# Kernel optimization log

Hardware: AMD Instinct MI355X
Metric: run time of the kernel (lower is better)

The kernel has to match this reference:

```python
import jax, jax.numpy as jnp
import numpy as np

S = (256, 256, 256)          # MRI volume shape
N = 50000                    # number of Gaussians
T = 16                       # fixed tile edge; covers max bbox width = 2*3*sigma_max*(S-1)+2 <= 15
SIG_MIN, SIG_MAX = 0.004, 0.008  # NN-distance-based sigma range (k_sigma=1)


def setup_inputs() -> dict:
    key = jax.random.key(0)
    k1, k2, k3 = jax.random.split(key, 3)
    centers = jax.random.uniform(k1, (N, 3), dtype=jnp.float32)
    sigmas = jax.random.uniform(k2, (N,), dtype=jnp.float32, minval=SIG_MIN, maxval=SIG_MAX)
    intensities = jax.random.uniform(k3, (N,), dtype=jnp.float32)
    return {"centers": centers, "sigmas": sigmas, "intensities": intensities}


def _splat(centers, sigmas, intensities):
    dt = centers.dtype
    scale = jnp.asarray([s - 1 for s in S], dtype=dt)            # (3,) == scale_factors
    shape_f = jnp.asarray(S, dtype=dt)                           # (3,)
    shape_i = jnp.asarray(S, dtype=jnp.int32)                    # (3,)

    center_vox = centers * scale                                 # (N,3) voxel-space centers
    cutoff = 3.0 * sigmas[:, None] * scale                       # (N,3)
    # original: min_idx = max(c-cut, 0).int(); max_idx = (min(c+cut, scale)+1).int(), clipped to S
    min_idx = jnp.floor(jnp.maximum(center_vox - cutoff, 0.0)).astype(jnp.int32)          # (N,3)
    max_idx = jnp.minimum(jnp.floor(jnp.minimum(center_vox + cutoff, scale)) + 1.0,
                          shape_f).astype(jnp.int32)             # (N,3), exclusive

    ar = jnp.arange(T, dtype=jnp.int32)
    idx = min_idx[:, :, None] + ar[None, None, :]                # (N,3,T) absolute voxel idx
    valid = idx < max_idx[:, :, None]                            # (N,3,T) inside variable bbox
    idx_c = jnp.minimum(idx, shape_i[None, :, None] - 1)         # clamp for safe gather/scatter

    # grid coordinate along axis a at voxel i is i/(S_a-1) (linspace(0,1,S_a))
    coord = idx_c.astype(dt) / scale[None, :, None]              # (N,3,T)
    d = coord - centers[:, :, None]                              # (N,3,T)
    d2 = (d[:, 0, :, None, None] ** 2
          + d[:, 1, None, :, None] ** 2
          + d[:, 2, None, None, :] ** 2)                         # (N,T,T,T)
    mask = (valid[:, 0, :, None, None]
            & valid[:, 1, None, :, None]
            & valid[:, 2, None, None, :])                        # (N,T,T,T)

    inv_two_sig2 = 0.5 / (sigmas * sigmas)                       # (N,)
    contrib = intensities[:, None, None, None] * jnp.exp(-d2 * inv_two_sig2[:, None, None, None])
    contrib = jnp.where(mask, contrib, jnp.zeros((), dt))        # (N,T,T,T)

    lin = (idx_c[:, 0, :, None, None] * (S[1] * S[2])
           + idx_c[:, 1, None, :, None] * S[2]
           + idx_c[:, 2, None, None, :])                         # (N,T,T,T) flat voxel index

    vol = jnp.zeros(S[0] * S[1] * S[2], dtype=dt)
    vol = vol.at[lin.reshape(-1)].add(contrib.reshape(-1))
    return vol.reshape(S)


def reference(centers, sigmas, intensities):
    return _splat(centers, sigmas, intensities)
```

## Files before the change

### kernel.cpp

```cpp
#include <hip/hip_runtime.h>


#define NTILE 32768
#define CAP   32
#define LOG2E 1.4426950408889634f

typedef unsigned long long ull;

struct __align__(16) Rec {
    float cy, cz, w2;
    unsigned meta;
    float ex[8];
};

__global__ __launch_bounds__(256) void bin_prep_kernel(
    const float* __restrict__ centers,
    const float* __restrict__ sigmas,
    const float* __restrict__ intens,
    int*  __restrict__ counts,
    Rec*  __restrict__ list,
    int N)
{
    int g = blockIdx.x * 256 + threadIdx.x;
    if (g >= N) return;
    int txi = blockIdx.y % 3;
    int tyi = blockIdx.y / 3;

    float cx = centers[3*g+0] * 255.0f;
    float cy = centers[3*g+1] * 255.0f;
    float cz = centers[3*g+2] * 255.0f;
    float sig = sigmas[g];
    float cut = 3.0f * sig * 255.0f;
    float cc[3] = {cx, cy, cz};
    int mn[3], mx[3];
    #pragma unroll
    for (int a = 0; a < 3; ++a) {
        mn[a] = (int)floorf(fmaxf(cc[a] - cut, 0.0f));
        mx[a] = (int)fminf(floorf(fminf(cc[a] + cut, 255.0f)) + 1.0f, 256.0f);
    }
    float s255 = sig * 255.0f;
    float w2 = -0.5f * LOG2E / (s255 * s255);
    float inten = intens[g];

    int t0x = mn[0] >> 3, t1x = (mx[0] - 1) >> 3;
    int t0y = mn[1] >> 3, t1y = (mx[1] - 1) >> 3;

    int tx = t0x + txi; if (tx > t1x) return;
    int ty = t0y + tyi; if (ty > t1y) return;

    int ox = tx << 3, oy = ty << 3;
    int lox = max(mn[0] - ox, 0), hix = min(mx[0] - ox, 8);
    int loy = max(mn[1] - oy, 0), hiy = min(mx[1] - oy, 8);

    float ex[8];
    #pragma unroll
    for (int i = 0; i < 8; ++i) {
        float d = (float)(ox + i) - cx;
        float v = exp2f(d * d * w2) * inten;
        ex[i] = (i >= lox && i < hix) ? v : 0.0f;
    }

    int tzc = ((int)cz) >> 3;
    int t = (tx << 10) | (ty << 5) | tzc;
    unsigned meta = (unsigned)mn[2] | ((unsigned)(mx[2] - 1) << 8)
                  | ((unsigned)loy << 16) | ((unsigned)hiy << 19);

    int slot = atomicAdd(&counts[t], 1);
    if (slot < CAP) {
        int4* p = (int4*)&list[(size_t)t * CAP + slot];
        p[0] = make_int4(__float_as_int(cy), __float_as_int(cz),
                         __float_as_int(w2), (int)meta);
        p[1] = make_int4(__float_as_int(ex[0]), __float_as_int(ex[1]),
                         __float_as_int(ex[2]), __float_as_int(ex[3]));
        p[2] = make_int4(__float_as_int(ex[4]), __float_as_int(ex[5]),
                         __float_as_int(ex[6]), __float_as_int(ex[7]));
    }
}

__global__ __launch_bounds__(256) void splat_main(
    const int*  __restrict__ counts,
    const Rec*  __restrict__ list,
    float* __restrict__ vol)
{
    __shared__ int4 sh[4][(3 * CAP + 2) * 3];

    int wid = threadIdx.x >> 6;
    int lane = threadIdx.x & 63;
    int t = __builtin_amdgcn_readfirstlane(blockIdx.x * 4 + wid);
    int ox = (t >> 10) << 3, oy = ((t >> 5) & 31) << 3, oz = (t & 31) << 3;
    int tz = t & 31;
    int ly = lane >> 3, lz = lane & 7;

    int c0 = (tz > 0)  ? counts[t - 1] : 0;  if (c0 > CAP) c0 = CAP;
    int c1 = counts[t];                       if (c1 > CAP) c1 = CAP;
    int c2 = (tz < 31) ? counts[t + 1] : 0;  if (c2 > CAP) c2 = CAP;
    int n01 = c0 + c1, ntot = n01 + c2;

    const int4* s0 = (const int4*)(list + (long)(t - 1) * CAP);
    const int4* s1 = (const int4*)(list + (long)t * CAP);
    const int4* s2 = (const int4*)(list + (long)(t + 1) * CAP);

    int e0 = 3 * c0, e1 = 3 * n01, etot = 3 * ntot;
    for (int k = lane; k < etot; k += 64) {
        const int4* src; int off;
        if (k < e0)      { src = s0; off = k; }
        else if (k < e1) { src = s1; off = k - e0; }
        else             { src = s2; off = k - e1; }
        sh[wid][k] = src[off];
    }

    float fy = (float)(oy + ly);
    float fz = (float)(oz + lz);

    float acc[8];
    #pragma unroll
    for (int i = 0; i < 8; ++i) acc[i] = 0.0f;

    const int4* P = sh[wid];

    int4 a0 = P[0], a1 = P[1], a2 = P[2];
    for (int k = 0; k < ntot; ++k) {
        int b = (k + 1) * 3;
        int4 b0 = P[b], b1 = P[b + 1], b2 = P[b + 2];

        unsigned meta = (unsigned)__builtin_amdgcn_readfirstlane(a0.w);
        int mnz  = (int)(meta & 0xFF);
        int mxzi = (int)((meta >> 8) & 0xFF);
        int loz = mnz - oz;      if (loz < 0) loz = 0;
        int hiz = mxzi + 1 - oz; if (hiz > 8) hiz = 8;
        if (loz < hiz) {
            int loy_ = (int)((meta >> 16) & 7);
            int hiy_ = (int)((meta >> 19) & 0xF);
            ull ym = ((~0ull) << (loy_ << 3)) & ((~0ull) >> (64 - (hiy_ << 3)));
            unsigned zpat = (0xFFu >> (8 - hiz)) & (0xFFu << loz);
            unsigned zrep = zpat * 0x01010101u;
            ull m = (((ull)zrep << 32) | (ull)zrep) & ym;

            float cyv = __int_as_float(a0.x), czv = __int_as_float(a0.y);
            float w2v = __int_as_float(a0.z);

            float dy = fy - cyv, dz = fz - czv;
            float e = exp2f(fmaf(dy, dy, dz * dz) * w2v);
            float em;
            asm("v_cndmask_b32 %0, 0, %1, %2" : "=v"(em) : "v"(e), "s"(m));

            acc[0] = fmaf(__int_as_float(a1.x), em, acc[0]);
            acc[1] = fmaf(__int_as_float(a1.y), em, acc[1]);
            acc[2] = fmaf(__int_as_float(a1.z), em, acc[2]);
            acc[3] = fmaf(__int_as_float(a1.w), em, acc[3]);
            acc[4] = fmaf(__int_as_float(a2.x), em, acc[4]);
            acc[5] = fmaf(__int_as_float(a2.y), em, acc[5]);
            acc[6] = fmaf(__int_as_float(a2.z), em, acc[6]);
            acc[7] = fmaf(__int_as_float(a2.w), em, acc[7]);
        }
        a0 = b0; a1 = b1; a2 = b2;
    }

    int ybase = ((oy + ly) << 8) + (oz + lz);
    #pragma unroll
    for (int i = 0; i < 8; ++i)
        vol[((ox + i) << 16) + ybase] = acc[i];
}

extern "C" void kernel_launch(void* const* d_in, const int* in_sizes, int n_in,
                              void* d_out, int out_size, void* d_ws, size_t ws_size,
                              hipStream_t stream) {
    const float* centers = (const float*)d_in[0];
    const float* sigmas  = (const float*)d_in[1];
    const float* intens  = (const float*)d_in[2];
    float* vol = (float*)d_out;
    const int N = in_sizes[1];

    char* ws = (char*)d_ws;
    int*  counts = (int*)ws;
    Rec*  list   = (Rec*)(ws + (size_t)NTILE * sizeof(int));

    hipMemsetAsync(counts, 0, (size_t)NTILE * sizeof(int), stream);

    int gblocks = (N + 255) / 256;
    bin_prep_kernel<<<dim3(gblocks, 9), 256, 0, stream>>>(centers, sigmas, intens,
                                                          counts, list, N);
    splat_main<<<NTILE / 4, 256, 0, stream>>>(counts, list, vol);
}
```

Baseline: 123.3 us.

## Process four z-tiles per wave with a ring buffer reusing neighbor bins

Each wavefront now handles a column of four consecutive z-tiles instead of one. It keeps a four-slot LDS ring of bin records, so each bin is loaded from global memory once and shared by up to three adjacent tiles rather than reloaded three times. Loads of the next bin are issued before computing the current tile, which overlaps global latency with compute. The cost is fewer waves in flight (grid shrinks by 4x) and more register and LDS pressure.

```diff
diff --git a/kernel.cpp b/kernel.cpp
--- a/kernel.cpp
+++ b/kernel.cpp
@@ -82,84 +82,116 @@
     const Rec*  __restrict__ list,
     float* __restrict__ vol)
 {
-    __shared__ int4 sh[4][(3 * CAP + 2) * 3];
+    __shared__ int4 ring[4][4][CAP * 3 + 3];
 
     int wid = threadIdx.x >> 6;
     int lane = threadIdx.x & 63;
-    int t = __builtin_amdgcn_readfirstlane(blockIdx.x * 4 + wid);
-    int ox = (t >> 10) << 3, oy = ((t >> 5) & 31) << 3, oz = (t & 31) << 3;
-    int tz = t & 31;
+    int u = __builtin_amdgcn_readfirstlane(blockIdx.x * 4 + wid);
+    int tx = u >> 8, ty = (u >> 3) & 31, zc = u & 7;
+    int colbase = (tx << 10) | (ty << 5);
+    int z0 = zc << 2;
+    int ox = tx << 3, oy = ty << 3;
     int ly = lane >> 3, lz = lane & 7;
-
-    int c0 = (tz > 0)  ? counts[t - 1] : 0;  if (c0 > CAP) c0 = CAP;
-    int c1 = counts[t];                       if (c1 > CAP) c1 = CAP;
-    int c2 = (tz < 31) ? counts[t + 1] : 0;  if (c2 > CAP) c2 = CAP;
-    int n01 = c0 + c1, ntot = n01 + c2;
-
-    const int4* s0 = (const int4*)(list + (long)(t - 1) * CAP);
-    const int4* s1 = (const int4*)(list + (long)t * CAP);
-    const int4* s2 = (const int4*)(list + (long)(t + 1) * CAP);
-
-    int e0 = 3 * c0, e1 = 3 * n01, etot = 3 * ntot;
-    for (int k = lane; k < etot; k += 64) {
-        const int4* src; int off;
-        if (k < e0)      { src = s0; off = k; }
-        else if (k < e1) { src = s1; off = k - e0; }
-        else             { src = s2; off = k - e1; }
-        sh[wid][k] = src[off];
-    }
-
     float fy = (float)(oy + ly);
-    float fz = (float)(oz + lz);
-
-    float acc[8];
-    #pragma unroll
-    for (int i = 0; i < 8; ++i) acc[i] = 0.0f;
-
-    const int4* P = sh[wid];
-
-    int4 a0 = P[0], a1 = P[1], a2 = P[2];
-    for (int k = 0; k < ntot; ++k) {
-        int b = (k + 1) * 3;
-        int4 b0 = P[b], b1 = P[b + 1], b2 = P[b + 2];
-
-        unsigned meta = (unsigned)__builtin_amdgcn_readfirstlane(a0.w);
-        int mnz  = (int)(meta & 0xFF);
-        int mxzi = (int)((meta >> 8) & 0xFF);
-        int loz = mnz - oz;      if (loz < 0) loz = 0;
-        int hiz = mxzi + 1 - oz; if (hiz > 8) hiz = 8;
-        if (loz < hiz) {
-            int loy_ = (int)((meta >> 16) & 7);
-            int hiy_ = (int)((meta >> 19) & 0xF);
-            ull ym = ((~0ull) << (loy_ << 3)) & ((~0ull) >> (64 - (hiy_ << 3)));
-            unsigned zpat = (0xFFu >> (8 - hiz)) & (0xFFu << loz);
-            unsigned zrep = zpat * 0x01010101u;
-            ull m = (((ull)zrep << 32) | (ull)zrep) & ym;
-
-            float cyv = __int_as_float(a0.x), czv = __int_as_float(a0.y);
-            float w2v = __int_as_float(a0.z);
-
-            float dy = fy - cyv, dz = fz - czv;
-            float e = exp2f(fmaf(dy, dy, dz * dz) * w2v);
-            float em;
-            asm("v_cndmask_b32 %0, 0, %1, %2" : "=v"(em) : "v"(e), "s"(m));
-
-            acc[0] = fmaf(__int_as_float(a1.x), em, acc[0]);
-            acc[1] = fmaf(__int_as_float(a1.y), em, acc[1]);
-            acc[2] = fmaf(__int_as_float(a1.z), em, acc[2]);
-            acc[3] = fmaf(__int_as_float(a1.w), em, acc[3]);
-            acc[4] = fmaf(__int_as_float(a2.x), em, acc[4]);
-            acc[5] = fmaf(__int_as_float(a2.y), em, acc[5]);
-            acc[6] = fmaf(__int_as_float(a2.z), em, acc[6]);
-            acc[7] = fmaf(__int_as_float(a2.w), em, acc[7]);
+
+    auto ldc = [&](int s) -> int {
+        if (s < 0 || s > 31) return 0;
+        int c = counts[colbase + s];
+        return c > CAP ? CAP : c;
+    };
+    int cA = ldc(z0 - 1), cB = ldc(z0), cC = ldc(z0 + 1);
+    int cD = ldc(z0 + 2), cE = ldc(z0 + 3), cF = ldc(z0 + 4);
+
+    auto stage_issue = [&](int s, int cnt, int4& v0, int4& v1) {
+        int ch = 3 * cnt;
+        const int4* src = (const int4*)(list + (size_t)(colbase + max(s, 0)) * CAP);
+        if (lane < ch)      v0 = src[lane];
+        if (lane + 64 < ch) v1 = src[lane + 64];
+    };
+    auto stage_write = [&](int rb, int cnt, int4 v0, int4 v1) {
+        int ch = 3 * cnt;
+        if (lane < ch)      ring[wid][rb][lane]      = v0;
+        if (lane + 64 < ch) ring[wid][rb][lane + 64] = v1;
+    };
+
+    auto proc = [&](int oz, float fz, int cnt, const int4* B, float (&acc)[8]) {
+        if (cnt == 0) return;
+        int4 a0 = B[0], a1 = B[1], a2 = B[2];
+        for (int k = 0; k < cnt; ++k) {
+            int b = (k + 1) * 3;
+            int4 b0 = B[b], b1 = B[b + 1], b2 = B[b + 2];
+
+            unsigned meta = (unsigned)__builtin_amdgcn_readfirstlane(a0.w);
+            int mnz  = (int)(meta & 0xFF);
+            int mxzi = (int)((meta >> 8) & 0xFF);
+            int loz = mnz - oz;      if (loz < 0) loz = 0;
+            int hiz = mxzi + 1 - oz; if (hiz > 8) hiz = 8;
+            if (loz < hiz) {
+                int loy_ = (int)((meta >> 16) & 7);
+                int hiy_ = (int)((meta >> 19) & 0xF);
+                ull ym = ((~0ull) << (loy_ << 3)) & ((~0ull) >> (64 - (hiy_ << 3)));
+                unsigned zpat = (0xFFu >> (8 - hiz)) & (0xFFu << loz);
+                unsigned zrep = zpat * 0x01010101u;
+                ull m = (((ull)zrep << 32) | (ull)zrep) & ym;
+
+                float cyv = __int_as_float(a0.x), czv = __int_as_float(a0.y);
+                float w2v = __int_as_float(a0.z);
+
+                float dy = fy - cyv, dz = fz - czv;
+                float e = exp2f(fmaf(dy, dy, dz * dz) * w2v);
+                float em;
+                asm("v_cndmask_b32 %0, 0, %1, %2" : "=v"(em) : "v"(e), "s"(m));
+
+                acc[0] = fmaf(__int_as_float(a1.x), em, acc[0]);
+                acc[1] = fmaf(__int_as_float(a1.y), em, acc[1]);
+                acc[2] = fmaf(__int_as_float(a1.z), em, acc[2]);
+                acc[3] = fmaf(__int_as_float(a1.w), em, acc[3]);
+                acc[4] = fmaf(__int_as_float(a2.x), em, acc[4]);
+                acc[5] = fmaf(__int_as_float(a2.y), em, acc[5]);
+                acc[6] = fmaf(__int_as_float(a2.z), em, acc[6]);
+                acc[7] = fmaf(__int_as_float(a2.w), em, acc[7]);
+            }
+            a0 = b0; a1 = b1; a2 = b2;
         }
-        a0 = b0; a1 = b1; a2 = b2;
-    }
-
-    int ybase = ((oy + ly) << 8) + (oz + lz);
-    #pragma unroll
-    for (int i = 0; i < 8; ++i)
-        vol[((ox + i) << 16) + ybase] = acc[i];
+    };
+
+    auto do_tile = [&](int tz, int cm, const int4* bm, int cc, const int4* bc,
+                       int cp, const int4* bp) {
+        int oz = tz << 3;
+        float fz = (float)(oz + lz);
+        float acc[8];
+        #pragma unroll
+        for (int i = 0; i < 8; ++i) acc[i] = 0.0f;
+        proc(oz, fz, cm, bm, acc);
+        proc(oz, fz, cc, bc, acc);
+        proc(oz, fz, cp, bp, acc);
+        int ybase = ((oy + ly) << 8) + (oz + lz);
+        #pragma unroll
+        for (int i = 0; i < 8; ++i)
+            vol[((ox + i) << 16) + ybase] = acc[i];
+    };
+
+    {
+        int4 av0 = {}, av1 = {}, bv0 = {}, bv1 = {}, cv0 = {}, cv1 = {};
+        stage_issue(z0 - 1, cA, av0, av1);
+        stage_issue(z0,     cB, bv0, bv1);
+        stage_issue(z0 + 1, cC, cv0, cv1);
+        stage_write(3, cA, av0, av1);
+        stage_write(0, cB, bv0, bv1);
+        stage_write(1, cC, cv0, cv1);
+    }
+
+    int4 s0v = {}, s1v = {};
+    stage_issue(z0 + 2, cD, s0v, s1v);
+    do_tile(z0 + 0, cA, ring[wid][3], cB, ring[wid][0], cC, ring[wid][1]);
+    stage_write(2, cD, s0v, s1v);
+    stage_issue(z0 + 3, cE, s0v, s1v);
+    do_tile(z0 + 1, cB, ring[wid][0], cC, ring[wid][1], cD, ring[wid][2]);
+    stage_write(3, cE, s0v, s1v);
+    stage_issue(z0 + 4, cF, s0v, s1v);
+    do_tile(z0 + 2, cC, ring[wid][1], cD, ring[wid][2], cE, ring[wid][3]);
+    stage_write(0, cF, s0v, s1v);
+    do_tile(z0 + 3, cD, ring[wid][2], cE, ring[wid][3], cF, ring[wid][0]);
 }
 
 extern "C" void kernel_launch(void* const* d_in, const int* in_sizes, int n_in,
@@ -180,5 +212,5 @@
     int gblocks = (N + 255) / 256;
     bin_prep_kernel<<<dim3(gblocks, 9), 256, 0, stream>>>(centers, sigmas, intens,
                                                           counts, list, N);
-    splat_main<<<NTILE / 4, 256, 0, stream>>>(counts, list, vol);
+    splat_main<<<8192 / 4, 256, 0, stream>>>(counts, list, vol);
 }
```

Result: slower. 133.8 us (+8.5%).

## Process four z-tiles per wave sharing Gaussian records and use raw v_exp

Applied to the files above, without the earlier changes.

Each wave now handles four consecutive 8-voxel z tiles instead of one. It loads the Gaussian records of six neighbouring z bins into shared memory once and reuses each record's y-term and metadata decode across all four tiles, which removes the redundant loads and decodes of neighbour bins. The exp2f calls are replaced with inline v_exp_f32, skipping the library's range handling. In exchange each wave uses more registers (32 accumulators) and more shared memory, and the grid is four times smaller, which may lower occupancy and parallelism.

```diff
diff --git a/kernel.cpp b/kernel.cpp
--- a/kernel.cpp
+++ b/kernel.cpp
@@ -6,6 +6,12 @@
 #define LOG2E 1.4426950408889634f
 
 typedef unsigned long long ull;
+
+__device__ __forceinline__ float fast_exp2(float x) {
+    float r;
+    asm("v_exp_f32 %0, %1" : "=v"(r) : "v"(x));
+    return r;
+}
 
 struct __align__(16) Rec {
     float cy, cz, w2;
@@ -56,7 +62,7 @@
     #pragma unroll
     for (int i = 0; i < 8; ++i) {
         float d = (float)(ox + i) - cx;
-        float v = exp2f(d * d * w2) * inten;
+        float v = fast_exp2(d * d * w2) * inten;
         ex[i] = (i >= lox && i < hix) ? v : 0.0f;
     }
 
@@ -82,84 +88,100 @@
     const Rec*  __restrict__ list,
     float* __restrict__ vol)
 {
-    __shared__ int4 sh[4][(3 * CAP + 2) * 3];
-
-    int wid = threadIdx.x >> 6;
+    __shared__ int4 sh[4][6 * CAP * 3 + 3];
+
+    int wid = __builtin_amdgcn_readfirstlane((int)(threadIdx.x >> 6));
     int lane = threadIdx.x & 63;
-    int t = __builtin_amdgcn_readfirstlane(blockIdx.x * 4 + wid);
-    int ox = (t >> 10) << 3, oy = ((t >> 5) & 31) << 3, oz = (t & 31) << 3;
-    int tz = t & 31;
+    int bid = __builtin_amdgcn_readfirstlane(blockIdx.x);
+    int col = bid >> 1, h = bid & 1;
+    int tx = col >> 5, ty = col & 31;
+    int tz0 = (h << 4) | (wid << 2);
+    int ox = tx << 3, oy = ty << 3, oz0 = tz0 << 3;
     int ly = lane >> 3, lz = lane & 7;
-
-    int c0 = (tz > 0)  ? counts[t - 1] : 0;  if (c0 > CAP) c0 = CAP;
-    int c1 = counts[t];                       if (c1 > CAP) c1 = CAP;
-    int c2 = (tz < 31) ? counts[t + 1] : 0;  if (c2 > CAP) c2 = CAP;
-    int n01 = c0 + c1, ntot = n01 + c2;
-
-    const int4* s0 = (const int4*)(list + (long)(t - 1) * CAP);
-    const int4* s1 = (const int4*)(list + (long)t * CAP);
-    const int4* s2 = (const int4*)(list + (long)(t + 1) * CAP);
-
-    int e0 = 3 * c0, e1 = 3 * n01, etot = 3 * ntot;
-    for (int k = lane; k < etot; k += 64) {
-        const int4* src; int off;
-        if (k < e0)      { src = s0; off = k; }
-        else if (k < e1) { src = s1; off = k - e0; }
-        else             { src = s2; off = k - e1; }
-        sh[wid][k] = src[off];
-    }
-
-    float fy = (float)(oy + ly);
-    float fz = (float)(oz + lz);
-
-    float acc[8];
-    #pragma unroll
-    for (int i = 0; i < 8; ++i) acc[i] = 0.0f;
+    int colbase = (tx << 10) | (ty << 5);
+
+    int cnt[6], off[6];
+    int run = 0, ntot = 0;
+    #pragma unroll
+    for (int s = 0; s < 6; ++s) {
+        int slot = tz0 - 1 + s;
+        int c = (slot >= 0 && slot < 32) ? counts[colbase + slot] : 0;
+        if (c > CAP) c = CAP;
+        cnt[s] = c; off[s] = run; run += 3 * c; ntot += c;
+    }
+
+    #pragma unroll
+    for (int s = 0; s < 6; ++s) {
+        const int4* src = (const int4*)(list + (size_t)(colbase + tz0 - 1 + s) * CAP);
+        int ch = 3 * cnt[s];
+        for (int j = lane; j < ch; j += 64)
+            sh[wid][off[s] + j] = src[j];
+    }
+
+    float fy  = (float)(oy + ly);
+    float fz0 = (float)(oz0 + lz);
+
+    float acc[4][8];
+    #pragma unroll
+    for (int j = 0; j < 4; ++j)
+        #pragma unroll
+        for (int i = 0; i < 8; ++i) acc[j][i] = 0.0f;
 
     const int4* P = sh[wid];
 
-    int4 a0 = P[0], a1 = P[1], a2 = P[2];
+    int4 A0 = P[0], A1 = P[1], A2 = P[2];
     for (int k = 0; k < ntot; ++k) {
         int b = (k + 1) * 3;
-        int4 b0 = P[b], b1 = P[b + 1], b2 = P[b + 2];
-
-        unsigned meta = (unsigned)__builtin_amdgcn_readfirstlane(a0.w);
+        int4 B0 = P[b], B1 = P[b + 1], B2 = P[b + 2];
+
+        unsigned meta = (unsigned)__builtin_amdgcn_readfirstlane(A0.w);
         int mnz  = (int)(meta & 0xFF);
         int mxzi = (int)((meta >> 8) & 0xFF);
-        int loz = mnz - oz;      if (loz < 0) loz = 0;
-        int hiz = mxzi + 1 - oz; if (hiz > 8) hiz = 8;
-        if (loz < hiz) {
-            int loy_ = (int)((meta >> 16) & 7);
-            int hiy_ = (int)((meta >> 19) & 0xF);
-            ull ym = ((~0ull) << (loy_ << 3)) & ((~0ull) >> (64 - (hiy_ << 3)));
-            unsigned zpat = (0xFFu >> (8 - hiz)) & (0xFFu << loz);
-            unsigned zrep = zpat * 0x01010101u;
-            ull m = (((ull)zrep << 32) | (ull)zrep) & ym;
-
-            float cyv = __int_as_float(a0.x), czv = __int_as_float(a0.y);
-            float w2v = __int_as_float(a0.z);
-
-            float dy = fy - cyv, dz = fz - czv;
-            float e = exp2f(fmaf(dy, dy, dz * dz) * w2v);
-            float em;
-            asm("v_cndmask_b32 %0, 0, %1, %2" : "=v"(em) : "v"(e), "s"(m));
-
-            acc[0] = fmaf(__int_as_float(a1.x), em, acc[0]);
-            acc[1] = fmaf(__int_as_float(a1.y), em, acc[1]);
-            acc[2] = fmaf(__int_as_float(a1.z), em, acc[2]);
-            acc[3] = fmaf(__int_as_float(a1.w), em, acc[3]);
-            acc[4] = fmaf(__int_as_float(a2.x), em, acc[4]);
-            acc[5] = fmaf(__int_as_float(a2.y), em, acc[5]);
-            acc[6] = fmaf(__int_as_float(a2.z), em, acc[6]);
-            acc[7] = fmaf(__int_as_float(a2.w), em, acc[7]);
+        int loy_ = (int)((meta >> 16) & 7);
+        int hiy_ = (int)((meta >> 19) & 0xF);
+        ull ym = ((~0ull) << (loy_ << 3)) & ((~0ull) >> (64 - (hiy_ << 3)));
+
+        float cyv = __int_as_float(A0.x), czv = __int_as_float(A0.y);
+        float w2v = __int_as_float(A0.z);
+        float dy = fy - cyv;
+        float dy2 = dy * dy;
+
+        #pragma unroll
+        for (int j = 0; j < 4; ++j) {
+            int ozj = oz0 + 8 * j;
+            int lozj = mnz - ozj;      if (lozj < 0) lozj = 0;
+            int hizj = mxzi + 1 - ozj; if (hizj > 8) hizj = 8;
+            if (lozj < hizj) {
+                unsigned zpat = (0xFFu >> (8 - hizj)) & (0xFFu << lozj);
+                unsigned zrep = zpat * 0x01010101u;
+                ull m = (((ull)zrep << 32) | (ull)zrep) & ym;
+
+                float dz = (fz0 + (float)(8 * j)) - czv;
+                float e = fast_exp2(fmaf(dz, dz, dy2) * w2v);
+                float em;
+                asm("v_cndmask_b32 %0, 0, %1, %2" : "=v"(em) : "v"(e), "s"(m));
+
+                acc[j][0] = fmaf(__int_as_float(A1.x), em, acc[j][0]);
+                acc[j][1] = fmaf(__int_as_float(A1.y), em, acc[j][1]);
+                acc[j][2] = fmaf(__int_as_float(A1.z), em, acc[j][2]);
+                acc[j][3] = fmaf(__int_as_float(A1.w), em, acc[j][3]);
+                acc[j][4] = fmaf(__int_as_float(A2.x), em, acc[j][4]);
+                acc[j][5] = fmaf(__int_as_float(A2.y), em, acc[j][5]);
+                acc[j][6] = fmaf(__int_as_float(A2.z), em, acc[j][6]);
+                acc[j][7] = fmaf(__int_as_float(A2.w), em, acc[j][7]);
+            }
         }
-        a0 = b0; a1 = b1; a2 = b2;
-    }
-
-    int ybase = ((oy + ly) << 8) + (oz + lz);
-    #pragma unroll
-    for (int i = 0; i < 8; ++i)
-        vol[((ox + i) << 16) + ybase] = acc[i];
+        A0 = B0; A1 = B1; A2 = B2;
+    }
+
+    int ybase = (oy + ly) << 8;
+    #pragma unroll
+    for (int j = 0; j < 4; ++j) {
+        int zabs = oz0 + 8 * j + lz;
+        #pragma unroll
+        for (int i = 0; i < 8; ++i)
+            vol[((ox + i) << 16) + ybase + zabs] = acc[j][i];
+    }
 }
 
 extern "C" void kernel_launch(void* const* d_in, const int* in_sizes, int n_in,
@@ -175,10 +197,10 @@
     int*  counts = (int*)ws;
     Rec*  list   = (Rec*)(ws + (size_t)NTILE * sizeof(int));
 
-    hipMemsetAsync(counts, 0, (size_t)NTILE * sizeof(int), stream);
+    (void)hipMemsetAsync(counts, 0, (size_t)NTILE * sizeof(int), stream);
 
     int gblocks = (N + 255) / 256;
     bin_prep_kernel<<<dim3(gblocks, 9), 256, 0, stream>>>(centers, sigmas, intens,
                                                           counts, list, N);
-    splat_main<<<NTILE / 4, 256, 0, stream>>>(counts, list, vol);
-}
+    splat_main<<<2048, 256, 0, stream>>>(counts, list, vol);
+}
```

New measurement: 132.7 us. 1.08x slower.
